# Kernel optimization log

Measured on AMD Instinct MI355X. Metric: run time of the kernel, lower is better.

## Reference

```python
import jax, jax.numpy as jnp
import numpy as np

H_HEADS = 8

def _conv1x1(x, w):
    # x: (b, C_in, H, W), w: (C_out, C_in, 1, 1)
    return jax.lax.conv_general_dilated(
        x, w, window_strides=(1, 1), padding='VALID',
        dimension_numbers=('NCHW', 'OIHW', 'NCHW'))

def setup_inputs() -> dict:
    key = jax.random.key(0)
    kx, kq, kk, kv = jax.random.split(key, 4)
    x = jax.random.normal(kx, (16, 256, 64, 64), dtype=jnp.float32)
    sc = 1.0 / np.sqrt(256.0)
    wq = jax.random.normal(kq, (256, 256, 1, 1), dtype=jnp.float32) * sc
    wk = jax.random.normal(kk, (256, 256, 1, 1), dtype=jnp.float32) * sc
    wv = jax.random.normal(kv, (256, 256, 1, 1), dtype=jnp.float32) * sc
    return {"x": x, "wq": wq, "wk": wk, "wv": wv}

def reference(x, wq, wk, wv):
    b, _, Hs, Ws = x.shape
    h = H_HEADS
    v = _conv1x1(x, wv)                      # (b, C, H, W)
    C = v.shape[1]
    d = C // h
    q = _conv1x1(x, wq).reshape(b, h, d, -1)  # (b, h, d, N)
    k = _conv1x1(x, wk).reshape(b, h, d, -1)
    vflat = v.reshape(b, h, d, -1)
    # channel-attention: contract over spatial N -> (b, h, d, d)
    scores = jnp.einsum('bhdn,bhen->bhde', q, k) / jnp.sqrt(jnp.float32(h))
    attn_weights = jax.nn.softmax(scores, axis=-1)
    attn = jnp.einsum('bhde,bhen->bhdn', attn_weights, vflat)  # (b, h, d, N)
    # ChannelShuffle(groups=h): (b, h, d, H, W) -> (b, d, h, H, W) -> (b, C, H, W)
    shuffled = attn.reshape(b, h, d, Hs, Ws).transpose(0, 2, 1, 3, 4).reshape(b, C, Hs, Ws)
    out = shuffled + v
    return (out, attn_weights)
```

## Files before the change

kernel.cpp:

```cpp
#include <hip/hip_runtime.h>
#include <hip/hip_bf16.h>
#include <stdint.h>

typedef __attribute__((ext_vector_type(4))) float f32x4;
typedef __attribute__((ext_vector_type(8))) short bf16x8;
typedef __attribute__((ext_vector_type(4))) short bf16x4;
typedef __attribute__((ext_vector_type(4))) unsigned int u32x4;

__device__ __forceinline__ unsigned short f2bf_rne(float f) {
  union { float f; unsigned int u; } v; v.f = f;
  unsigned int r = v.u + 0x7FFFu + ((v.u >> 16) & 1u);
  return (unsigned short)(r >> 16);
}
__device__ __forceinline__ float bf2f(unsigned short s) {
  union { float f; unsigned int u; } v; v.u = ((unsigned int)s) << 16;
  return v.f;
}

__global__ __launch_bounds__(1024) void k_gram(const float* __restrict__ x,
                                               float* __restrict__ Gpart) {
  __shared__ __align__(16) unsigned char lds[256 * 128];
  const int b = blockIdx.y;
  const int n0 = blockIdx.x << 8;
  const int t = threadIdx.x;
  const int lane = t & 63;
  const int w = t >> 6;
  const int wm = (w >> 2) << 6;
  const int wn = (w & 3) << 6;
  const int c_ld = t >> 2;
  const int noct = t & 3;
  const int lrow = lane & 15;
  const int lkg = lane >> 4;

  f32x4 acc[4][4];
#pragma unroll
  for (int i = 0; i < 4; i++)
#pragma unroll
    for (int j = 0; j < 4; j++) acc[i][j] = (f32x4){0.f, 0.f, 0.f, 0.f};

  const float* gx = x + (((size_t)(b * 256 + c_ld)) << 12) + n0 + (noct << 3);
  f32x4 v0 = *(const f32x4*)(gx);
  f32x4 v1 = *(const f32x4*)(gx + 4);

  for (int sub = 0; sub < 8; sub++) {
    float vv[8] = {v0[0], v0[1], v0[2], v0[3], v1[0], v1[1], v1[2], v1[3]};
    unsigned short hi[8], lo[8];
#pragma unroll
    for (int j = 0; j < 8; j++) {
      hi[j] = f2bf_rne(vv[j]);
      lo[j] = f2bf_rne(vv[j] - bf2f(hi[j]));
    }
    u32x4 hw = {(unsigned)hi[0] | ((unsigned)hi[1] << 16),
                (unsigned)hi[2] | ((unsigned)hi[3] << 16),
                (unsigned)hi[4] | ((unsigned)hi[5] << 16),
                (unsigned)hi[6] | ((unsigned)hi[7] << 16)};
    u32x4 lw = {(unsigned)lo[0] | ((unsigned)lo[1] << 16),
                (unsigned)lo[2] | ((unsigned)lo[3] << 16),
                (unsigned)lo[4] | ((unsigned)lo[5] << 16),
                (unsigned)lo[6] | ((unsigned)lo[7] << 16)};

    __syncthreads();
    const int swz = (c_ld & 7) << 4;
    *(u32x4*)(lds + c_ld * 128 + (((noct << 4)) ^ swz)) = hw;
    *(u32x4*)(lds + c_ld * 128 + ((64 + (noct << 4)) ^ swz)) = lw;
    __syncthreads();

    if (sub < 7) {
      v0 = *(const f32x4*)(gx + ((sub + 1) << 5));
      v1 = *(const f32x4*)(gx + ((sub + 1) << 5) + 4);
    }

    bf16x8 bh[4], bl[4];
#pragma unroll
    for (int nf = 0; nf < 4; nf++) {
      int col = wn + (nf << 4) + lrow;
      int cs = (col & 7) << 4;
      bh[nf] = *(const bf16x8*)(lds + col * 128 + (((lkg << 4)) ^ cs));
      bl[nf] = *(const bf16x8*)(lds + col * 128 + ((64 + (lkg << 4)) ^ cs));
    }
#pragma unroll
    for (int mf = 0; mf < 4; mf++) {
      int row = wm + (mf << 4) + lrow;
      int rs = (row & 7) << 4;
      bf16x8 ah = *(const bf16x8*)(lds + row * 128 + (((lkg << 4)) ^ rs));
      bf16x8 al = *(const bf16x8*)(lds + row * 128 + ((64 + (lkg << 4)) ^ rs));
#pragma unroll
      for (int nf = 0; nf < 4; nf++) {
        acc[mf][nf] = __builtin_amdgcn_mfma_f32_16x16x32_bf16(ah, bh[nf], acc[mf][nf], 0, 0, 0);
        acc[mf][nf] = __builtin_amdgcn_mfma_f32_16x16x32_bf16(ah, bl[nf], acc[mf][nf], 0, 0, 0);
        acc[mf][nf] = __builtin_amdgcn_mfma_f32_16x16x32_bf16(al, bh[nf], acc[mf][nf], 0, 0, 0);
      }
    }
  }

  if (wm <= wn) {
    float* Gp = Gpart + (((size_t)(blockIdx.x * 16 + b)) << 16);
#pragma unroll
    for (int mf = 0; mf < 4; mf++)
#pragma unroll
      for (int nf = 0; nf < 4; nf++) {
        int col = wn + (nf << 4) + lrow;
#pragma unroll
        for (int r = 0; r < 4; r++) {
          int row = wm + (mf << 4) + (lkg << 2) + r;
          Gp[row * 256 + col] = acc[mf][nf][r];
        }
      }
  }
}

__global__ __launch_bounds__(256) void k_reduce(const float* __restrict__ Gpart,
                                                float* __restrict__ G) {
  __shared__ float tl[64][68];
  const int bx = blockIdx.x;
  const int b = bx / 10;
  int tp = bx % 10;
  int i = 0;
  while (tp >= 4 - i) { tp -= 4 - i; ++i; }
  const int j = i + tp;
  const int t = threadIdx.x;
  const int r = t >> 2, cg = t & 3;

  f32x4 s[4];
#pragma unroll
  for (int q = 0; q < 4; q++) s[q] = (f32x4){0.f, 0.f, 0.f, 0.f};
  const float* src = Gpart + ((size_t)b << 16) + (size_t)(i * 64 + r) * 256 + j * 64 + cg * 16;
  for (int ch = 0; ch < 16; ch++) {
    const float* p = src + (((size_t)ch) << 20);
#pragma unroll
    for (int q = 0; q < 4; q++) s[q] += *(const f32x4*)(p + (q << 2));
  }
  float* dst = G + ((size_t)b << 16) + (size_t)(i * 64 + r) * 256 + j * 64 + cg * 16;
#pragma unroll
  for (int q = 0; q < 4; q++) *(f32x4*)(dst + (q << 2)) = s[q];

  if (i != j) {
#pragma unroll
    for (int q = 0; q < 4; q++) *(f32x4*)&tl[r][cg * 16 + (q << 2)] = s[q];
    __syncthreads();
    const int c2 = t >> 2, g2 = t & 3;
    float vals[16];
#pragma unroll
    for (int q = 0; q < 16; q++) vals[q] = tl[g2 * 16 + q][c2];
    float* d2 = G + ((size_t)b << 16) + (size_t)(j * 64 + c2) * 256 + i * 64 + g2 * 16;
#pragma unroll
    for (int q = 0; q < 4; q++) {
      f32x4 vv = {vals[4 * q], vals[4 * q + 1], vals[4 * q + 2], vals[4 * q + 3]};
      *(f32x4*)(d2 + (q << 2)) = vv;
    }
  }
}

__global__ __launch_bounds__(512) void k_scores(const float* __restrict__ wq,
                                                const float* __restrict__ wk,
                                                const float* __restrict__ wv,
                                                const float* __restrict__ G,
                                                float* __restrict__ attn,
                                                unsigned short* __restrict__ Wout) {
  __shared__ float part[8][16][256];
  const int h = blockIdx.x, b = blockIdx.y, dg = blockIdx.z;
  const int t = threadIdx.x, lane = t & 63;
  const int wu = __builtin_amdgcn_readfirstlane(t >> 6);

  const float* wqrow = wq + (size_t)(h * 32 + dg * 16) * 256 + wu * 32;
  f32x4 tp[16];
#pragma unroll
  for (int d = 0; d < 16; d++) tp[d] = (f32x4){0.f, 0.f, 0.f, 0.f};

  const float* Gb = G + ((size_t)b << 16) + (size_t)(wu * 32) * 256 + (lane << 2);
  for (int s = 0; s < 32; s++) {
    f32x4 g = *(const f32x4*)(Gb + s * 256);
#pragma unroll
    for (int d = 0; d < 16; d++)
      tp[d] += g * wqrow[d * 256 + s];
  }
#pragma unroll
  for (int d = 0; d < 16; d++)
    *(f32x4*)&part[wu][d][lane << 2] = tp[d];
  __syncthreads();

#pragma unroll
  for (int u = 0; u < 2; u++) {
    int o = t * 2 + u;
    int d = o >> 6, q = (o & 63) << 2;
    f32x4 s = *(f32x4*)&part[0][d][q];
#pragma unroll
    for (int w2 = 1; w2 < 8; w2++) s += *(f32x4*)&part[w2][d][q];
    *(f32x4*)&part[0][d][q] = s;
  }
  __syncthreads();
  const float* Tb = &part[0][0][0];

  const int dls = t >> 5, es = t & 31;
  f32x4 sa = {0.f, 0.f, 0.f, 0.f};
  const float* Tr = Tb + dls * 256;
  const float* wkr = wk + (size_t)(h * 32 + es) * 256;
  for (int c4 = 0; c4 < 64; c4++)
    sa += *(const f32x4*)(Tr + (c4 << 2)) * *(const f32x4*)(wkr + (c4 << 2));
  float s = (sa[0] + sa[1] + sa[2] + sa[3]) * 0.35355339059327379f;

  float m = s;
#pragma unroll
  for (int off = 1; off < 32; off <<= 1) m = fmaxf(m, __shfl_xor(m, off));
  float p = expf(s - m);
  float su = p;
#pragma unroll
  for (int off = 1; off < 32; off <<= 1) su += __shfl_xor(su, off);
  float a = p / su;
  attn[(((b * 8 + h) * 32) + dg * 16 + dls) * 32 + es] = a;

  f32x4 o0 = {0.f, 0.f, 0.f, 0.f}, o1 = {0.f, 0.f, 0.f, 0.f};
  const float* wvh = wv + (size_t)(h * 32) * 256 + (lane << 2);
#pragma unroll
  for (int e = 0; e < 32; e++) {
    float a0 = __shfl(a, e);
    float a1 = __shfl(a, 32 + e);
    f32x4 vv = *(const f32x4*)(wvh + e * 256);
    o0 += vv * a0;
    o1 += vv * a1;
  }
  const int d0 = dg * 16 + 2 * wu;
  const int co0 = d0 * 8 + h, co1 = (d0 + 1) * 8 + h;
  o0 += *(const f32x4*)(wv + (size_t)co0 * 256 + (lane << 2));
  o1 += *(const f32x4*)(wv + (size_t)co1 * 256 + (lane << 2));
  bf16x4 p0, p1;
#pragma unroll
  for (int j = 0; j < 4; j++) {
    p0[j] = (short)f2bf_rne(o0[j]);
    p1[j] = (short)f2bf_rne(o1[j]);
  }
  *(bf16x4*)(Wout + ((size_t)(b * 256 + co0) << 8) + (lane << 2)) = p0;
  *(bf16x4*)(Wout + ((size_t)(b * 256 + co1) << 8) + (lane << 2)) = p1;
}

__global__ __launch_bounds__(512) void k_out(const float* __restrict__ x,
                                             const unsigned short* __restrict__ Wout,
                                             float* __restrict__ out) {
  __shared__ __align__(16) unsigned short Bt[4096];
  const int b = blockIdx.y;
  const int nb = blockIdx.x << 7;
  const int t = threadIdx.x;
  const int lane = t & 63;
  const int w = t >> 6;
  const int wm = (w >> 1) << 6;
  const int wn = (w & 1) << 6;
  const int lrow = lane & 15;
  const int lkg = lane >> 4;

  f32x4 acc[4][4];
#pragma unroll
  for (int i = 0; i < 4; i++)
#pragma unroll
    for (int j = 0; j < 4; j++) acc[i][j] = (f32x4){0.f, 0.f, 0.f, 0.f};

  const int pos = lane >> 3;
  const int cblk = 2 * (pos & 3) + (pos >> 2);
  const int ctil = cblk * 4 + ((lane & 7) >> 1);
  const int noff = (lane & 1) << 3;
  const float* gxb = x + (((size_t)b) << 20) + (size_t)ctil * 4096 + nb + (w << 4) + noff;
  const unsigned int bt0 = (unsigned int)(uintptr_t)(&Bt[0]);

  f32x4 xa = *(const f32x4*)(gxb);
  f32x4 xb = *(const f32x4*)(gxb + 4);

  for (int kt = 0; kt < 8; kt++) {
    __syncthreads();
    bf16x8 pk;
#pragma unroll
    for (int j = 0; j < 4; j++) {
      pk[j] = (short)f2bf_rne(xa[j]);
      pk[4 + j] = (short)f2bf_rne(xb[j]);
    }
    *(bf16x8*)(Bt + (w << 9) + (lane << 3)) = pk;
    __syncthreads();

    if (kt < 7) {
      const float* nx = gxb + (((size_t)(kt + 1)) << 17);
      xa = *(const f32x4*)(nx);
      xb = *(const f32x4*)(nx + 4);
    }

    bf16x8 afr[4];
    const unsigned short* wrow = Wout + (((size_t)(b * 256)) << 8) + kt * 32 + (lkg << 3);
#pragma unroll
    for (int mf = 0; mf < 4; mf++) {
      int co = wm + (mf << 4) + lrow;
      afr[mf] = *(const bf16x8*)(wrow + ((size_t)co << 8));
    }

    bf16x4 t0[4], t1[4];
#pragma unroll
    for (int nf = 0; nf < 4; nf++) {
      unsigned int base = bt0 + (unsigned int)((((wn >> 4) + nf)) << 10) + (lane << 3);
      asm volatile("ds_read_b64_tr_b16 %0, %1" : "=v"(t0[nf]) : "v"(base) : "memory");
      asm volatile("ds_read_b64_tr_b16 %0, %1 offset:512" : "=v"(t1[nf]) : "v"(base) : "memory");
    }
    asm volatile("s_waitcnt lgkmcnt(0)" ::: "memory");
    __builtin_amdgcn_sched_barrier(0);

    bf16x8 bfr[4];
#pragma unroll
    for (int nf = 0; nf < 4; nf++) {
      bfr[nf][0] = t0[nf][0]; bfr[nf][1] = t0[nf][1];
      bfr[nf][2] = t0[nf][2]; bfr[nf][3] = t0[nf][3];
      bfr[nf][4] = t1[nf][0]; bfr[nf][5] = t1[nf][1];
      bfr[nf][6] = t1[nf][2]; bfr[nf][7] = t1[nf][3];
    }
#pragma unroll
    for (int mf = 0; mf < 4; mf++)
#pragma unroll
      for (int nf = 0; nf < 4; nf++)
        acc[mf][nf] = __builtin_amdgcn_mfma_f32_16x16x32_bf16(afr[mf], bfr[nf], acc[mf][nf], 0, 0, 0);
  }

  float* ob = out + (((size_t)b) << 20) + nb;
#pragma unroll
  for (int mf = 0; mf < 4; mf++)
#pragma unroll
    for (int nf = 0; nf < 4; nf++) {
      int col = wn + (nf << 4) + lrow;
#pragma unroll
      for (int r = 0; r < 4; r++) {
        int row = wm + (mf << 4) + (lkg << 2) + r;
        ob[((size_t)row << 12) + col] = acc[mf][nf][r];
      }
    }
}

extern "C" void kernel_launch(void* const* d_in, const int* in_sizes, int n_in,
                              void* d_out, int out_size, void* d_ws, size_t ws_size,
                              hipStream_t stream) {
  const float* x = (const float*)d_in[0];
  const float* wq = (const float*)d_in[1];
  const float* wk = (const float*)d_in[2];
  const float* wv = (const float*)d_in[3];
  float* out = (float*)d_out;
  float* attn = out + (size_t)16 * 256 * 4096;

  float* Gpart = out;

  char* ws = (char*)d_ws;
  float* G = (float*)ws;
  unsigned short* Wout = (unsigned short*)(ws + (4 << 20));

  k_gram<<<dim3(16, 16), dim3(1024), 0, stream>>>(x, Gpart);
  k_reduce<<<dim3(160), dim3(256), 0, stream>>>(Gpart, G);
  k_scores<<<dim3(8, 16, 2), dim3(512), 0, stream>>>(wq, wk, wv, G, attn, Wout);
  k_out<<<dim3(32, 16), dim3(512), 0, stream>>>(x, Wout, out);
}
```

Measured before the change: 103.8 us.

## Fuse Gram reduction into k_gram via last-block atomic and double-buffer LDS

Removes the separate k_reduce launch. The last k_gram block to finish for each batch, detected with an atomic counter and thread fences, now sums the 16 partial Gram matrices and writes the symmetric G. Both k_gram and k_out switch to double-buffered LDS, which drops one __syncthreads per iteration. In exchange this adds a memset launch and a tail phase that runs serially on one block per batch, and the larger LDS footprint may reduce occupancy.

```diff
diff --git a/kernel.cpp b/kernel.cpp
--- a/kernel.cpp
+++ b/kernel.cpp
@@ -18,8 +18,10 @@
 }
 
 __global__ __launch_bounds__(1024) void k_gram(const float* __restrict__ x,
-                                               float* __restrict__ Gpart) {
-  __shared__ __align__(16) unsigned char lds[256 * 128];
+                                               float* __restrict__ Gpart,
+                                               float* __restrict__ G,
+                                               int* __restrict__ cnt) {
+  __shared__ __align__(16) unsigned char lds[2][32768];
   const int b = blockIdx.y;
   const int n0 = blockIdx.x << 8;
   const int t = threadIdx.x;
@@ -43,6 +45,7 @@
   f32x4 v1 = *(const f32x4*)(gx + 4);
 
   for (int sub = 0; sub < 8; sub++) {
+    unsigned char* buf = lds[sub & 1];
     float vv[8] = {v0[0], v0[1], v0[2], v0[3], v1[0], v1[1], v1[2], v1[3]};
     unsigned short hi[8], lo[8];
 #pragma unroll
@@ -58,11 +61,9 @@
                 (unsigned)lo[2] | ((unsigned)lo[3] << 16),
                 (unsigned)lo[4] | ((unsigned)lo[5] << 16),
                 (unsigned)lo[6] | ((unsigned)lo[7] << 16)};
-
-    __syncthreads();
     const int swz = (c_ld & 7) << 4;
-    *(u32x4*)(lds + c_ld * 128 + (((noct << 4)) ^ swz)) = hw;
-    *(u32x4*)(lds + c_ld * 128 + ((64 + (noct << 4)) ^ swz)) = lw;
+    *(u32x4*)(buf + c_ld * 128 + (((noct << 4)) ^ swz)) = hw;
+    *(u32x4*)(buf + c_ld * 128 + ((64 + (noct << 4)) ^ swz)) = lw;
     __syncthreads();
 
     if (sub < 7) {
@@ -75,15 +76,15 @@
     for (int nf = 0; nf < 4; nf++) {
       int col = wn + (nf << 4) + lrow;
       int cs = (col & 7) << 4;
-      bh[nf] = *(const bf16x8*)(lds + col * 128 + (((lkg << 4)) ^ cs));
-      bl[nf] = *(const bf16x8*)(lds + col * 128 + ((64 + (lkg << 4)) ^ cs));
+      bh[nf] = *(const bf16x8*)(buf + col * 128 + (((lkg << 4)) ^ cs));
+      bl[nf] = *(const bf16x8*)(buf + col * 128 + ((64 + (lkg << 4)) ^ cs));
     }
 #pragma unroll
     for (int mf = 0; mf < 4; mf++) {
       int row = wm + (mf << 4) + lrow;
       int rs = (row & 7) << 4;
-      bf16x8 ah = *(const bf16x8*)(lds + row * 128 + (((lkg << 4)) ^ rs));
-      bf16x8 al = *(const bf16x8*)(lds + row * 128 + ((64 + (lkg << 4)) ^ rs));
+      bf16x8 ah = *(const bf16x8*)(buf + row * 128 + (((lkg << 4)) ^ rs));
+      bf16x8 al = *(const bf16x8*)(buf + row * 128 + ((64 + (lkg << 4)) ^ rs));
 #pragma unroll
       for (int nf = 0; nf < 4; nf++) {
         acc[mf][nf] = __builtin_amdgcn_mfma_f32_16x16x32_bf16(ah, bh[nf], acc[mf][nf], 0, 0, 0);
@@ -107,46 +108,37 @@
         }
       }
   }
-}
-
-__global__ __launch_bounds__(256) void k_reduce(const float* __restrict__ Gpart,
-                                                float* __restrict__ G) {
-  __shared__ float tl[64][68];
-  const int bx = blockIdx.x;
-  const int b = bx / 10;
-  int tp = bx % 10;
-  int i = 0;
-  while (tp >= 4 - i) { tp -= 4 - i; ++i; }
-  const int j = i + tp;
-  const int t = threadIdx.x;
-  const int r = t >> 2, cg = t & 3;
-
-  f32x4 s[4];
-#pragma unroll
-  for (int q = 0; q < 4; q++) s[q] = (f32x4){0.f, 0.f, 0.f, 0.f};
-  const float* src = Gpart + ((size_t)b << 16) + (size_t)(i * 64 + r) * 256 + j * 64 + cg * 16;
-  for (int ch = 0; ch < 16; ch++) {
-    const float* p = src + (((size_t)ch) << 20);
-#pragma unroll
-    for (int q = 0; q < 4; q++) s[q] += *(const f32x4*)(p + (q << 2));
-  }
-  float* dst = G + ((size_t)b << 16) + (size_t)(i * 64 + r) * 256 + j * 64 + cg * 16;
-#pragma unroll
-  for (int q = 0; q < 4; q++) *(f32x4*)(dst + (q << 2)) = s[q];
-
-  if (i != j) {
-#pragma unroll
-    for (int q = 0; q < 4; q++) *(f32x4*)&tl[r][cg * 16 + (q << 2)] = s[q];
-    __syncthreads();
-    const int c2 = t >> 2, g2 = t & 3;
-    float vals[16];
-#pragma unroll
-    for (int q = 0; q < 16; q++) vals[q] = tl[g2 * 16 + q][c2];
-    float* d2 = G + ((size_t)b << 16) + (size_t)(j * 64 + c2) * 256 + i * 64 + g2 * 16;
-#pragma unroll
-    for (int q = 0; q < 4; q++) {
-      f32x4 vv = {vals[4 * q], vals[4 * q + 1], vals[4 * q + 2], vals[4 * q + 3]};
-      *(f32x4*)(d2 + (q << 2)) = vv;
+
+  __threadfence();
+  __syncthreads();
+  __shared__ int lastf;
+  if (t == 0) lastf = (atomicAdd(cnt + b, 1) == 15);
+  __syncthreads();
+  if (!lastf) return;
+  __threadfence();
+
+  float* tl = (float*)lds;
+  const int rr = t >> 4, c4 = t & 15;
+  const int TI[10] = {0, 0, 0, 0, 1, 1, 1, 2, 2, 3};
+  const int TJ[10] = {0, 1, 2, 3, 1, 2, 3, 2, 3, 3};
+#pragma unroll
+  for (int tp = 0; tp < 10; tp++) {
+    const int i = TI[tp], j = TJ[tp];
+    const float* src = Gpart + ((size_t)b << 16) + (size_t)(i * 64 + rr) * 256 + j * 64 + (c4 << 2);
+    f32x4 s = *(const f32x4*)(src);
+#pragma unroll
+    for (int ch = 1; ch < 16; ch++)
+      s += *(const f32x4*)(src + (((size_t)ch) << 20));
+    *(f32x4*)(G + ((size_t)b << 16) + (size_t)(i * 64 + rr) * 256 + j * 64 + (c4 << 2)) = s;
+    if (i != j) {
+#pragma unroll
+      for (int q = 0; q < 4; q++) tl[rr * 73 + c4 * 4 + q] = s[q];
+      __syncthreads();
+      f32x4 m;
+#pragma unroll
+      for (int q = 0; q < 4; q++) m[q] = tl[(c4 * 4 + q) * 73 + rr];
+      *(f32x4*)(G + ((size_t)b << 16) + (size_t)(j * 64 + rr) * 256 + i * 64 + (c4 << 2)) = m;
+      __syncthreads();
     }
   }
 }
@@ -236,7 +228,7 @@
 __global__ __launch_bounds__(512) void k_out(const float* __restrict__ x,
                                              const unsigned short* __restrict__ Wout,
                                              float* __restrict__ out) {
-  __shared__ __align__(16) unsigned short Bt[4096];
+  __shared__ __align__(16) unsigned short Bt[2][4096];
   const int b = blockIdx.y;
   const int nb = blockIdx.x << 7;
   const int t = threadIdx.x;
@@ -258,20 +250,20 @@
   const int ctil = cblk * 4 + ((lane & 7) >> 1);
   const int noff = (lane & 1) << 3;
   const float* gxb = x + (((size_t)b) << 20) + (size_t)ctil * 4096 + nb + (w << 4) + noff;
-  const unsigned int bt0 = (unsigned int)(uintptr_t)(&Bt[0]);
+  const unsigned int bt0 = (unsigned int)(uintptr_t)(&Bt[0][0]);
 
   f32x4 xa = *(const f32x4*)(gxb);
   f32x4 xb = *(const f32x4*)(gxb + 4);
 
   for (int kt = 0; kt < 8; kt++) {
-    __syncthreads();
+    const int p = kt & 1;
     bf16x8 pk;
 #pragma unroll
     for (int j = 0; j < 4; j++) {
       pk[j] = (short)f2bf_rne(xa[j]);
       pk[4 + j] = (short)f2bf_rne(xb[j]);
     }
-    *(bf16x8*)(Bt + (w << 9) + (lane << 3)) = pk;
+    *(bf16x8*)(&Bt[p][(w << 9) + (lane << 3)]) = pk;
     __syncthreads();
 
     if (kt < 7) {
@@ -291,7 +283,8 @@
     bf16x4 t0[4], t1[4];
 #pragma unroll
     for (int nf = 0; nf < 4; nf++) {
-      unsigned int base = bt0 + (unsigned int)((((wn >> 4) + nf)) << 10) + (lane << 3);
+      unsigned int base = bt0 + (unsigned int)(p << 13) +
+                          (unsigned int)((((wn >> 4) + nf)) << 10) + (lane << 3);
       asm volatile("ds_read_b64_tr_b16 %0, %1" : "=v"(t0[nf]) : "v"(base) : "memory");
       asm volatile("ds_read_b64_tr_b16 %0, %1 offset:512" : "=v"(t1[nf]) : "v"(base) : "memory");
     }
@@ -342,9 +335,10 @@
   char* ws = (char*)d_ws;
   float* G = (float*)ws;
   unsigned short* Wout = (unsigned short*)(ws + (4 << 20));
-
-  k_gram<<<dim3(16, 16), dim3(1024), 0, stream>>>(x, Gpart);
-  k_reduce<<<dim3(160), dim3(256), 0, stream>>>(Gpart, G);
+  int* cnt = (int*)(ws + (6 << 20));
+
+  hipMemsetAsync(cnt, 0, 64, stream);
+  k_gram<<<dim3(16, 16), dim3(1024), 0, stream>>>(x, Gpart, G, cnt);
   k_scores<<<dim3(8, 16, 2), dim3(512), 0, stream>>>(wq, wk, wv, G, attn, Wout);
   k_out<<<dim3(32, 16), dim3(512), 0, stream>>>(x, Wout, out);
 }
```

Result: slower. 292.8 us (+182.0%).
